# Kernel optimization log

Measured on AMD Instinct MI355X. Metric: run time of the kernel, lower is better.

The kernel has to match this reference:

```python
import jax, jax.numpy as jnp
import numpy as np

B, S, D = 4, 2048, 512
H, HD, RL = 8, 64, 64   # nheads, head_dim = D//H, rl_dim
TEMPER = 1.0
BETA = 1.0
SLOPE = 0.01  # LeakyReLU negative slope
LN_EPS = 1e-5


def setup_inputs() -> dict:
    key = jax.random.key(0)
    ks = jax.random.split(key, 12)
    scale = 0.02
    return {
        "h":   jax.random.normal(ks[0], (B, S, D), dtype=jnp.float32),
        "rh":  jax.random.normal(ks[1], (B, S, RL), dtype=jnp.float32),
        "Wl":  jax.random.normal(ks[2], (D, D), dtype=jnp.float32) * scale,   # linear_l (in,out)
        "Wr":  jax.random.normal(ks[3], (D, D), dtype=jnp.float32) * scale,   # linear_r
        "al":  jax.random.normal(ks[4], (HD,), dtype=jnp.float32) * scale,    # att_l: Linear(head_dim,1)
        "ar":  jax.random.normal(ks[5], (HD,), dtype=jnp.float32) * scale,    # att_r
        "Wrs": jax.random.normal(ks[6], (RL, RL * H), dtype=jnp.float32) * scale,  # r_source
        "Wrt": jax.random.normal(ks[7], (RL, RL * H), dtype=jnp.float32) * scale,  # r_target
        "Wf":  jax.random.normal(ks[8], (D, D), dtype=jnp.float32) * scale,   # linear_final
        "ln_g": jnp.ones((D,), dtype=jnp.float32),
        "ln_b": jnp.zeros((D,), dtype=jnp.float32),
    }


def _layer_norm(x, g, b):
    mu = jnp.mean(x, axis=-1, keepdims=True)
    var = jnp.mean(jnp.square(x - mu), axis=-1, keepdims=True)
    return (x - mu) * jax.lax.rsqrt(var + LN_EPS) * g + b


def reference(h, rh, Wl, Wr, al, ar, Wrs, Wrt, Wf, ln_g, ln_b):
    leaky = lambda x: jnp.where(x >= 0, x, SLOPE * x)
    # projections -> [B, H, S, HD]
    fl = (h @ Wl).reshape(B, S, H, HD).transpose(0, 2, 1, 3)
    fr = (h @ Wr).reshape(B, S, H, HD).transpose(0, 2, 1, 3)
    # additive attention logits: [B,H,S,1] + [B,H,1,S]
    sl = jnp.einsum('bhsd,d->bhs', leaky(fl), al)
    sr = jnp.einsum('bhsd,d->bhs', leaky(fr), ar)
    score = sl[:, :, :, None] + sr[:, :, None, :]
    # relation-embedding bilinear bias: r_k @ r_q -> [B,H,S,S]
    r_k = (rh @ Wrs).reshape(B, S, H, RL).transpose(0, 2, 1, 3)   # [B,H,S,RL]
    r_q = (rh @ Wrt).reshape(B, S, H, RL).transpose(0, 2, 3, 1)   # [B,H,RL,S]
    score = score + BETA * jnp.einsum('bhsr,bhrt->bhst', r_k, r_q)
    score = jax.nn.softmax(score / TEMPER, axis=-1)
    # context and output projection (dropout = 0 -> identity)
    context = jnp.einsum('bhst,bhtd->bhsd', score, fr)
    h_sa = context.transpose(0, 2, 1, 3).reshape(B, S, H * HD)
    fh = h_sa @ Wf
    return _layer_norm(h + fh, ln_g, ln_b)
```

## Files before the change

### kernel.cpp

```cpp
#include <hip/hip_runtime.h>
#include <math.h>

#define B_ 4
#define S_ 2048
#define D_ 512
#define H_ 8
#define HD_ 64
#define RL_ 64
#define LN_EPS 1e-5f
#define SLOPE 0.01f
#define LOG2E 1.4426950408889634f

typedef __attribute__((ext_vector_type(8))) __bf16 bf16x8;
typedef __attribute__((ext_vector_type(4))) float f32x4;

__device__ __forceinline__ float leaky(float x) { return x >= 0.f ? x : SLOPE * x; }

__device__ __forceinline__ ushort f2bf(float f) {
    union { float f; unsigned u; } v; v.f = f;
    unsigned r = v.u + 0x7fffu + ((v.u >> 16) & 1u);
    return (ushort)(r >> 16);
}
__device__ __forceinline__ unsigned fbits(float f) {
    union { float f; unsigned u; } v; v.f = f; return v.u;
}

__device__ __forceinline__ void g2lds16(const void* g, void* l) {
    __builtin_amdgcn_global_load_lds(
        (const __attribute__((address_space(1))) void*)(uintptr_t)g,
        (__attribute__((address_space(3))) void*)(uintptr_t)l, 16, 0, 0);
}

__global__ __launch_bounds__(256) void prep(
    const float* __restrict__ h, const float* __restrict__ rh,
    const float* __restrict__ Wr, const float* __restrict__ Wf,
    const float* __restrict__ Wrs, const float* __restrict__ Wrt,
    ushort* __restrict__ hb, ushort* __restrict__ rhb,
    ushort* __restrict__ WrT, ushort* __restrict__ WfT,
    ushort* __restrict__ WrsT, ushort* __restrict__ WrtT)
{
    const int bx = blockIdx.x, tid = threadIdx.x;
    if (bx < 4608) {
        const float* in = (bx < 4096) ? h : rh;
        ushort* o = (bx < 4096) ? hb : rhb;
        const int i = (bx < 4096 ? bx : bx - 4096) * 256 + tid;
        const float4 v = ((const float4*)in)[i];
        ushort4 u; u.x = f2bf(v.x); u.y = f2bf(v.y); u.z = f2bf(v.z); u.w = f2bf(v.w);
        ((ushort4*)o)[i] = u;
        return;
    }
    __shared__ float TS[64][65];
    int t = bx - 4608;
    const float* in; ushort* out; int K, tk, tn;
    if (t < 64)       { in = Wr;  out = WrT;  K = 512; tk = t & 7; tn = t >> 3; }
    else if (t < 128) { in = Wf;  out = WfT;  K = 512; t -= 64; tk = t & 7; tn = t >> 3; }
    else if (t < 136) { in = Wrs; out = WrsT; K = 64;  tk = 0; tn = t - 128; }
    else              { in = Wrt; out = WrtT; K = 64;  tk = 0; tn = t - 136; }
    const int k0 = tk * 64, n0 = tn * 64;
    const int r = tid >> 4, c4 = (tid & 15) * 4;
    #pragma unroll
    for (int p = 0; p < 4; ++p) {
        const int row = r + 16 * p;
        const float4 v = *(const float4*)(in + (size_t)(k0 + row) * 512 + n0 + c4);
        TS[row][c4] = v.x; TS[row][c4 + 1] = v.y;
        TS[row][c4 + 2] = v.z; TS[row][c4 + 3] = v.w;
    }
    __syncthreads();
    #pragma unroll
    for (int p = 0; p < 4; ++p) {
        const int nn = r + 16 * p;
        ushort4 o;
        o.x = f2bf(TS[c4 + 0][nn]); o.y = f2bf(TS[c4 + 1][nn]);
        o.z = f2bf(TS[c4 + 2][nn]); o.w = f2bf(TS[c4 + 3][nn]);
        *(ushort4*)(out + (size_t)(n0 + nn) * K + k0 + c4) = o;
    }
}

__global__ __launch_bounds__(256) void proj(
    const ushort* __restrict__ hb, const ushort* __restrict__ rhb,
    const ushort* __restrict__ WrT, const ushort* __restrict__ WrsT,
    const ushort* __restrict__ WrtT,
    ushort* __restrict__ frT, ushort* __restrict__ rkw, ushort* __restrict__ rqw,
    float* __restrict__ sred, const float* __restrict__ ar)
{
    __shared__ ushort As[2][64 * 32];
    __shared__ ushort Bs[2][128 * 32];

    const int tid = threadIdx.x;
    const int lane = tid & 63, w = tid >> 6;
    const int ln = lane & 15, quad = lane >> 4;
    const int wm = w >> 1, wn = w & 1;
    const int m0 = blockIdx.x * 64, n0 = blockIdx.y * 128;
    const int z = blockIdx.z;

    const ushort* A; const ushort* wt; ushort* co; float scl; int K;
    if (z == 0)      { A = hb;  wt = WrT;  co = frT; scl = LOG2E; K = 512; }
    else if (z == 1) { A = rhb; wt = WrsT; co = rkw; scl = LOG2E; K = 64; }
    else             { A = rhb; wt = WrtT; co = rqw; scl = 1.0f;  K = 64; }

    const int srA = tid >> 2;
    const int lchA = ((lane & 3) - (srA >> 1)) & 3;
    const ushort* AgB = A + (size_t)(m0 + srA) * K + lchA * 8;
    const int srB = w * 32 + (lane >> 2);
    const int lchB = ((lane & 3) - (srB >> 1)) & 3;
    const ushort* BgB0 = wt + (size_t)(n0 + srB) * K + lchB * 8;
    const ushort* BgB1 = BgB0 + (size_t)16 * K;
    const int aoff = tid * 8;
    const int boff = srB * 32 + (lane & 3) * 8;
    const int pc = (quad + (ln >> 1)) & 3;

    g2lds16(AgB, &As[0][aoff]);
    g2lds16(BgB0, &Bs[0][boff]);
    g2lds16(BgB1, &Bs[0][boff + 512]);

    f32x4 acc[2][4] = {};
    int buf = 0;
    for (int k0 = 0; k0 < K; k0 += 32) {
        __syncthreads();
        if (k0 + 32 < K) {
            g2lds16(AgB + k0 + 32, &As[buf ^ 1][aoff]);
            g2lds16(BgB0 + k0 + 32, &Bs[buf ^ 1][boff]);
            g2lds16(BgB1 + k0 + 32, &Bs[buf ^ 1][boff + 512]);
        }
        bf16x8 af[2], bfr[4];
        #pragma unroll
        for (int mi = 0; mi < 2; ++mi)
            af[mi] = *(const bf16x8*)&As[buf][(wm * 32 + mi * 16 + ln) * 32 + pc * 8];
        #pragma unroll
        for (int ni = 0; ni < 4; ++ni)
            bfr[ni] = *(const bf16x8*)&Bs[buf][(wn * 64 + ni * 16 + ln) * 32 + pc * 8];
        #pragma unroll
        for (int mi = 0; mi < 2; ++mi)
            #pragma unroll
            for (int ni = 0; ni < 4; ++ni)
                acc[mi][ni] = __builtin_amdgcn_mfma_f32_16x16x32_bf16(
                    af[mi], bfr[ni], acc[mi][ni], 0, 0, 0);
        buf ^= 1;
    }

    const int head = blockIdx.y * 2 + wn;
    const int b = m0 >> 11;
    const size_t bh = (size_t)b * H_ + head;
    if (z == 0) {
        #pragma unroll
        for (int mi = 0; mi < 2; ++mi) {
            const int s = (m0 & (S_ - 1)) + wm * 32 + mi * 16 + quad * 4;
            #pragma unroll
            for (int ni = 0; ni < 4; ++ni) {
                const int d = ni * 16 + ln;
                ushort4 o;
                o.x = f2bf(acc[mi][ni][0]); o.y = f2bf(acc[mi][ni][1]);
                o.z = f2bf(acc[mi][ni][2]); o.w = f2bf(acc[mi][ni][3]);
                *(ushort4*)(co + (bh * 64 + d) * S_ + s) = o;
            }
        }
        float a4[4];
        #pragma unroll
        for (int ni = 0; ni < 4; ++ni) a4[ni] = ar[ni * 16 + ln];
        #pragma unroll
        for (int mi = 0; mi < 2; ++mi) {
            const int s = (m0 & (S_ - 1)) + wm * 32 + mi * 16 + quad * 4;
            #pragma unroll
            for (int r = 0; r < 4; ++r) {
                float v = 0.f;
                #pragma unroll
                for (int ni = 0; ni < 4; ++ni)
                    v += leaky(acc[mi][ni][r]) * a4[ni];
                #pragma unroll
                for (int off = 8; off; off >>= 1) v += __shfl_xor(v, off, 16);
                if (ln == 0) sred[bh * S_ + s + r] = v * scl;
            }
        }
    } else {
        #pragma unroll
        for (int mi = 0; mi < 2; ++mi) {
            const int s = (m0 & (S_ - 1)) + wm * 32 + mi * 16 + quad * 4;
            #pragma unroll
            for (int ni = 0; ni < 4; ++ni) {
                const int d = ni * 16 + ln;
                #pragma unroll
                for (int r = 0; r < 4; ++r)
                    co[(bh * S_ + s + r) * 64 + d] = f2bf(acc[mi][ni][r] * scl);
            }
        }
    }
}

__global__ __launch_bounds__(256, 2) void attn_mfma(
    const ushort* __restrict__ frT, const ushort* __restrict__ rk,
    const ushort* __restrict__ rq, const float* __restrict__ sr,
    ushort* __restrict__ hsa)
{
    __shared__ ushort RQ[2][64][64];
    __shared__ ushort FT[2][64][64];
    __shared__ ushort PS[8][16][64];

    const int tid = threadIdx.x;
    const int w = tid >> 6;
    const int lane = tid & 63;
    const int ln = lane & 15;
    const int quad = lane >> 4;
    const int b = blockIdx.z, h = blockIdx.y, q0 = blockIdx.x * 128;
    const size_t bh = (size_t)b * H_ + h;

    bf16x8 a[2][2];
    #pragma unroll
    for (int qs = 0; qs < 2; ++qs) {
        const ushort* p = rk + ((bh * S_ + q0 + 32 * w + 16 * qs + ln) << 6);
        a[qs][0] = *(const bf16x8*)(p + quad * 8);
        a[qs][1] = *(const bf16x8*)(p + 32 + quad * 8);
    }

    const ushort* rq_g = rq + (bh * S_ << 6);
    const ushort* ft_g = frT + (size_t)bh * 64 * S_;
    const float* srp = sr + bh * S_;

    const int rl = lane >> 3;
    const int pg = lane & 7;
    const int row_b = w * 16 + rl;
    const int sgF = (pg - rl) & 7;
    const int sgR0 = (pg - 4 * w - (rl >> 2)) & 7;
    const int sgR1 = (pg - 4 * w - 2 - (rl >> 2)) & 7;

    #define STAGE(BUF, t0)                                                    \
        {                                                                     \
            g2lds16(rq_g + ((size_t)((t0) + row_b) << 6) + sgR0 * 8,          \
                    &RQ[BUF][row_b][pg * 8]);                                 \
            g2lds16(rq_g + ((size_t)((t0) + row_b + 8) << 6) + sgR1 * 8,      \
                    &RQ[BUF][row_b + 8][pg * 8]);                             \
            g2lds16(ft_g + (size_t)row_b * S_ + (t0) + sgF * 8,               \
                    &FT[BUF][row_b][pg * 8]);                                 \
            g2lds16(ft_g + (size_t)(row_b + 8) * S_ + (t0) + sgF * 8,         \
                    &FT[BUF][row_b + 8][pg * 8]);                             \
        }

    const ushort* rqrA = &RQ[0][0][0] + 4 * ln * 64 + ((quad + ln) & 7) * 8;
    const ushort* rqrB = &RQ[0][0][0] + 4 * ln * 64 + ((quad + 4 + ln) & 7) * 8;
    const ushort* ftrA = &FT[0][0][0] + ln * 64 + ((quad + ln) & 7) * 8;
    const ushort* ftrB = &FT[0][0][0] + ln * 64 + ((quad + 4 + ln) & 7) * 8;
    ushort* sb[2];
    sb[0] = &PS[w * 2][0][0]; sb[1] = &PS[w * 2 + 1][0][0];
    int wr_off[4];
    #pragma unroll
    for (int r = 0; r < 4; ++r) {
        const int prow = quad * 4 + r;
        wr_off[r] = prow * 64 + (((ln >> 1) + prow) & 7) * 8 + (ln & 1) * 4;
    }
    const int rd0 = ln * 64 + ((quad + ln) & 7) * 8;
    const int rd1 = ln * 64 + ((quad + 4 + ln) & 7) * 8;

    STAGE(0, 0)
    __syncthreads();

    float lsum[2][4] = {};
    f32x4 ctx[2][4] = {};

    for (int t0 = 0; t0 < S_; t0 += 128) {
        #pragma unroll
        for (int half = 0; half < 2; ++half) {
            const int tc = t0 + 64 * half;
            if (tc + 64 < S_) {
                if (half == 0) STAGE(1, tc + 64)
                else           STAGE(0, tc + 64)
            }
            const float4 srv = *(const float4*)(srp + tc + 4 * ln);

            f32x4 sc[2][4];
            #pragma unroll
            for (int jb = 0; jb < 4; ++jb) {
                const bf16x8 b0 = *(const bf16x8*)(rqrA + half * 4096 + jb * 64);
                const bf16x8 b1 = *(const bf16x8*)(rqrB + half * 4096 + jb * 64);
                #pragma unroll
                for (int qs = 0; qs < 2; ++qs) {
                    f32x4 t = {0.f, 0.f, 0.f, 0.f};
                    t = __builtin_amdgcn_mfma_f32_16x16x32_bf16(a[qs][0], b0, t, 0, 0, 0);
                    t = __builtin_amdgcn_mfma_f32_16x16x32_bf16(a[qs][1], b1, t, 0, 0, 0);
                    sc[qs][jb] = t;
                }
            }

            #pragma unroll
            for (int qs = 0; qs < 2; ++qs)
                #pragma unroll
                for (int r = 0; r < 4; ++r) {
                    const float p0 = __builtin_amdgcn_exp2f(sc[qs][0][r] + srv.x);
                    const float p1 = __builtin_amdgcn_exp2f(sc[qs][1][r] + srv.y);
                    const float p2 = __builtin_amdgcn_exp2f(sc[qs][2][r] + srv.z);
                    const float p3 = __builtin_amdgcn_exp2f(sc[qs][3][r] + srv.w);
                    lsum[qs][r] += (p0 + p1) + (p2 + p3);
                    const unsigned lo = (fbits(p0) >> 16) | (fbits(p1) & 0xffff0000u);
                    const unsigned hi = (fbits(p2) >> 16) | (fbits(p3) & 0xffff0000u);
                    *(uint2*)(sb[qs] + wr_off[r]) = make_uint2(lo, hi);
                }

            const bf16x8 pa00 = *(const bf16x8*)(sb[0] + rd0);
            const bf16x8 pa01 = *(const bf16x8*)(sb[0] + rd1);
            const bf16x8 pa10 = *(const bf16x8*)(sb[1] + rd0);
            const bf16x8 pa11 = *(const bf16x8*)(sb[1] + rd1);
            #pragma unroll
            for (int jb = 0; jb < 4; ++jb) {
                const bf16x8 fb0 = *(const bf16x8*)(ftrA + half * 4096 + jb * 1024);
                const bf16x8 fb1 = *(const bf16x8*)(ftrB + half * 4096 + jb * 1024);
                ctx[0][jb] = __builtin_amdgcn_mfma_f32_16x16x32_bf16(pa00, fb0, ctx[0][jb], 0, 0, 0);
                ctx[0][jb] = __builtin_amdgcn_mfma_f32_16x16x32_bf16(pa01, fb1, ctx[0][jb], 0, 0, 0);
                ctx[1][jb] = __builtin_amdgcn_mfma_f32_16x16x32_bf16(pa10, fb0, ctx[1][jb], 0, 0, 0);
                ctx[1][jb] = __builtin_amdgcn_mfma_f32_16x16x32_bf16(pa11, fb1, ctx[1][jb], 0, 0, 0);
            }

            __syncthreads();
        }
    }

    #pragma unroll
    for (int qs = 0; qs < 2; ++qs)
        #pragma unroll
        for (int r = 0; r < 4; ++r) {
            float l = lsum[qs][r];
            #pragma unroll
            for (int off = 8; off; off >>= 1) l += __shfl_xor(l, off, 16);
            const float inv = 1.f / l;
            const int q = q0 + 32 * w + 16 * qs + quad * 4 + r;
            ushort* orow = hsa + (size_t)(b * S_ + q) * D_ + h * 64;
            #pragma unroll
            for (int jb = 0; jb < 4; ++jb)
                orow[16 * jb + ln] = f2bf(ctx[qs][jb][r] * inv);
        }
}

__global__ __launch_bounds__(256) void gemm_out(
    const ushort* __restrict__ A, const ushort* __restrict__ WT,
    float* __restrict__ C)
{
    __shared__ ushort As[2][64 * 32];
    __shared__ ushort Bs[2][128 * 32];

    const int tid = threadIdx.x;
    const int lane = tid & 63, w = tid >> 6;
    const int ln = lane & 15, quad = lane >> 4;
    const int wm = w >> 1, wn = w & 1;
    const int m0 = blockIdx.x * 64, n0 = blockIdx.y * 128;
    const int K = 512;

    const int srA = tid >> 2;
    const int lchA = ((lane & 3) - (srA >> 1)) & 3;
    const ushort* AgB = A + (size_t)(m0 + srA) * K + lchA * 8;
    const int srB = w * 32 + (lane >> 2);
    const int lchB = ((lane & 3) - (srB >> 1)) & 3;
    const ushort* BgB0 = WT + (size_t)(n0 + srB) * K + lchB * 8;
    const ushort* BgB1 = BgB0 + (size_t)16 * K;
    const int aoff = tid * 8;
    const int boff = srB * 32 + (lane & 3) * 8;
    const int pc = (quad + (ln >> 1)) & 3;

    g2lds16(AgB, &As[0][aoff]);
    g2lds16(BgB0, &Bs[0][boff]);
    g2lds16(BgB1, &Bs[0][boff + 512]);

    f32x4 acc[2][4] = {};
    int buf = 0;
    for (int k0 = 0; k0 < K; k0 += 32) {
        __syncthreads();
        if (k0 + 32 < K) {
            g2lds16(AgB + k0 + 32, &As[buf ^ 1][aoff]);
            g2lds16(BgB0 + k0 + 32, &Bs[buf ^ 1][boff]);
            g2lds16(BgB1 + k0 + 32, &Bs[buf ^ 1][boff + 512]);
        }
        bf16x8 af[2], bfr[4];
        #pragma unroll
        for (int mi = 0; mi < 2; ++mi)
            af[mi] = *(const bf16x8*)&As[buf][(wm * 32 + mi * 16 + ln) * 32 + pc * 8];
        #pragma unroll
        for (int ni = 0; ni < 4; ++ni)
            bfr[ni] = *(const bf16x8*)&Bs[buf][(wn * 64 + ni * 16 + ln) * 32 + pc * 8];
        #pragma unroll
        for (int mi = 0; mi < 2; ++mi)
            #pragma unroll
            for (int ni = 0; ni < 4; ++ni)
                acc[mi][ni] = __builtin_amdgcn_mfma_f32_16x16x32_bf16(
                    af[mi], bfr[ni], acc[mi][ni], 0, 0, 0);
        buf ^= 1;
    }

    #pragma unroll
    for (int mi = 0; mi < 2; ++mi) {
        const int row = m0 + wm * 32 + mi * 16 + quad * 4;
        #pragma unroll
        for (int ni = 0; ni < 4; ++ni) {
            const int col = n0 + wn * 64 + ni * 16 + ln;
            #pragma unroll
            for (int r = 0; r < 4; ++r)
                C[(size_t)(row + r) * 512 + col] = acc[mi][ni][r];
        }
    }
}

__global__ __launch_bounds__(256) void ln_kernel(
    const float* __restrict__ h, const float* __restrict__ fh,
    const float* __restrict__ g, const float* __restrict__ bb,
    float* __restrict__ out)
{
    const int row = blockIdx.x, tid = threadIdx.x;
    const float* hp = h + (size_t)row * 512;
    const float* fp = fh + (size_t)row * 512;
    const float x0 = hp[tid] + fp[tid];
    const float x1 = hp[tid + 256] + fp[tid + 256];
    __shared__ float red[4];

    float s = x0 + x1;
    #pragma unroll
    for (int off = 32; off; off >>= 1) s += __shfl_xor(s, off, 64);
    if ((tid & 63) == 0) red[tid >> 6] = s;
    __syncthreads();
    const float mu = (red[0] + red[1] + red[2] + red[3]) * (1.f / 512.f);

    const float d0 = x0 - mu, d1 = x1 - mu;
    float v = d0 * d0 + d1 * d1;
    #pragma unroll
    for (int off = 32; off; off >>= 1) v += __shfl_xor(v, off, 64);
    __syncthreads();
    if ((tid & 63) == 0) red[tid >> 6] = v;
    __syncthreads();
    const float var = (red[0] + red[1] + red[2] + red[3]) * (1.f / 512.f);
    const float inv = rsqrtf(var + LN_EPS);

    out[(size_t)row * 512 + tid] = d0 * inv * g[tid] + bb[tid];
    out[(size_t)row * 512 + tid + 256] = d1 * inv * g[tid + 256] + bb[tid + 256];
}

extern "C" void kernel_launch(void* const* d_in, const int* in_sizes, int n_in,
                              void* d_out, int out_size, void* d_ws, size_t ws_size,
                              hipStream_t stream)
{
    const float* h   = (const float*)d_in[0];
    const float* rh  = (const float*)d_in[1];
    const float* Wr  = (const float*)d_in[3];
    const float* ar  = (const float*)d_in[5];
    const float* Wrs = (const float*)d_in[6];
    const float* Wrt = (const float*)d_in[7];
    const float* Wf  = (const float*)d_in[8];
    const float* lng = (const float*)d_in[9];
    const float* lnb = (const float*)d_in[10];
    float* out = (float*)d_out;
    char* wsb  = (char*)d_ws;

    const size_t MB = (size_t)1 << 20;
    ushort* hb   = (ushort*)(wsb);
    ushort* rhb  = (ushort*)(wsb + 8 * MB);
    ushort* WrT  = (ushort*)(wsb + 9 * MB);
    ushort* WfT  = (ushort*)(wsb + 9 * MB + 512 * 1024);
    ushort* WrsT = (ushort*)(wsb + 10 * MB);
    ushort* WrtT = (ushort*)(wsb + 10 * MB + 64 * 1024);
    ushort* frT  = (ushort*)(wsb + 11 * MB);
    ushort* rkw  = (ushort*)(wsb + 19 * MB);
    ushort* rqw  = (ushort*)(wsb + 27 * MB);
    float*  sr   = (float*) (wsb + 35 * MB);
    ushort* hsab = (ushort*)(wsb + 36 * MB);
    float*  fh   = (float*) (wsb + 44 * MB);

    dim3 blk(256);
    prep<<<dim3(4752), blk, 0, stream>>>(h, rh, Wr, Wf, Wrs, Wrt,
                                         hb, rhb, WrT, WfT, WrsT, WrtT);
    proj<<<dim3(128, 4, 3), blk, 0, stream>>>(hb, rhb, WrT, WrsT, WrtT,
                                              frT, rkw, rqw, sr, ar);
    attn_mfma<<<dim3(S_ / 128, H_, B_), blk, 0, stream>>>(frT, rkw, rqw, sr, hsab);
    gemm_out<<<dim3(128, 4), blk, 0, stream>>>(hsab, WfT, fh);
    ln_kernel<<<dim3(B_ * S_), blk, 0, stream>>>(h, fh, lng, lnb, out);
}
```

Before: 175.5 us.

## Fuse output GEMM with residual LayerNorm; load A fragments directly from global

Replaces the separate output-projection GEMM and LayerNorm kernels with one kernel where each block computes 32 full rows of 512 columns, adds the residual and does the row-normalisation in registers with a shared-memory reduction. This removes the fp32 intermediate write and read of fh and one launch. It also loads A-operand MFMA fragments straight from global memory into registers, in both proj and the new kernel, dropping the A shared-memory staging. The trade-off is a grid of only 256 large blocks with big LDS use and launch_bounds(…,1), which lowers occupancy. Variance is now computed as E[x²]−mu² in one pass, which is slightly less numerically robust.

```diff
diff --git a/kernel.cpp b/kernel.cpp
--- a/kernel.cpp
+++ b/kernel.cpp
@@ -83,7 +83,6 @@
     ushort* __restrict__ frT, ushort* __restrict__ rkw, ushort* __restrict__ rqw,
     float* __restrict__ sred, const float* __restrict__ ar)
 {
-    __shared__ ushort As[2][64 * 32];
     __shared__ ushort Bs[2][128 * 32];
 
     const int tid = threadIdx.x;
@@ -98,34 +97,33 @@
     else if (z == 1) { A = rhb; wt = WrsT; co = rkw; scl = LOG2E; K = 64; }
     else             { A = rhb; wt = WrtT; co = rqw; scl = 1.0f;  K = 64; }
 
-    const int srA = tid >> 2;
-    const int lchA = ((lane & 3) - (srA >> 1)) & 3;
-    const ushort* AgB = A + (size_t)(m0 + srA) * K + lchA * 8;
     const int srB = w * 32 + (lane >> 2);
     const int lchB = ((lane & 3) - (srB >> 1)) & 3;
     const ushort* BgB0 = wt + (size_t)(n0 + srB) * K + lchB * 8;
     const ushort* BgB1 = BgB0 + (size_t)16 * K;
-    const int aoff = tid * 8;
     const int boff = srB * 32 + (lane & 3) * 8;
     const int pc = (quad + (ln >> 1)) & 3;
 
-    g2lds16(AgB, &As[0][aoff]);
+    const ushort* Ar0 = A + (size_t)(m0 + wm * 32 + ln) * K + quad * 8;
+    const ushort* Ar1 = A + (size_t)(m0 + wm * 32 + 16 + ln) * K + quad * 8;
+
     g2lds16(BgB0, &Bs[0][boff]);
     g2lds16(BgB1, &Bs[0][boff + 512]);
+    bf16x8 a_cur[2], a_nxt[2];
+    a_cur[0] = *(const bf16x8*)Ar0;
+    a_cur[1] = *(const bf16x8*)Ar1;
 
     f32x4 acc[2][4] = {};
     int buf = 0;
     for (int k0 = 0; k0 < K; k0 += 32) {
         __syncthreads();
         if (k0 + 32 < K) {
-            g2lds16(AgB + k0 + 32, &As[buf ^ 1][aoff]);
             g2lds16(BgB0 + k0 + 32, &Bs[buf ^ 1][boff]);
             g2lds16(BgB1 + k0 + 32, &Bs[buf ^ 1][boff + 512]);
-        }
-        bf16x8 af[2], bfr[4];
-        #pragma unroll
-        for (int mi = 0; mi < 2; ++mi)
-            af[mi] = *(const bf16x8*)&As[buf][(wm * 32 + mi * 16 + ln) * 32 + pc * 8];
+            a_nxt[0] = *(const bf16x8*)(Ar0 + k0 + 32);
+            a_nxt[1] = *(const bf16x8*)(Ar1 + k0 + 32);
+        }
+        bf16x8 bfr[4];
         #pragma unroll
         for (int ni = 0; ni < 4; ++ni)
             bfr[ni] = *(const bf16x8*)&Bs[buf][(wn * 64 + ni * 16 + ln) * 32 + pc * 8];
@@ -134,7 +132,8 @@
             #pragma unroll
             for (int ni = 0; ni < 4; ++ni)
                 acc[mi][ni] = __builtin_amdgcn_mfma_f32_16x16x32_bf16(
-                    af[mi], bfr[ni], acc[mi][ni], 0, 0, 0);
+                    a_cur[mi], bfr[ni], acc[mi][ni], 0, 0, 0);
+        a_cur[0] = a_nxt[0]; a_cur[1] = a_nxt[1];
         buf ^= 1;
     }
 
@@ -327,104 +326,112 @@
         }
 }
 
-__global__ __launch_bounds__(256) void gemm_out(
+__global__ __launch_bounds__(256, 1) void gemm_ln(
     const ushort* __restrict__ A, const ushort* __restrict__ WT,
-    float* __restrict__ C)
+    const float* __restrict__ h, const float* __restrict__ g,
+    const float* __restrict__ bb, float* __restrict__ out)
 {
-    __shared__ ushort As[2][64 * 32];
-    __shared__ ushort Bs[2][128 * 32];
+    __shared__ ushort Bs[2][512 * 32];
+    __shared__ float red[32][8];
 
     const int tid = threadIdx.x;
     const int lane = tid & 63, w = tid >> 6;
     const int ln = lane & 15, quad = lane >> 4;
-    const int wm = w >> 1, wn = w & 1;
-    const int m0 = blockIdx.x * 64, n0 = blockIdx.y * 128;
-    const int K = 512;
-
-    const int srA = tid >> 2;
-    const int lchA = ((lane & 3) - (srA >> 1)) & 3;
-    const ushort* AgB = A + (size_t)(m0 + srA) * K + lchA * 8;
-    const int srB = w * 32 + (lane >> 2);
-    const int lchB = ((lane & 3) - (srB >> 1)) & 3;
-    const ushort* BgB0 = WT + (size_t)(n0 + srB) * K + lchB * 8;
-    const ushort* BgB1 = BgB0 + (size_t)16 * K;
-    const int aoff = tid * 8;
-    const int boff = srB * 32 + (lane & 3) * 8;
-    const int pc = (quad + (ln >> 1)) & 3;
-
-    g2lds16(AgB, &As[0][aoff]);
-    g2lds16(BgB0, &Bs[0][boff]);
-    g2lds16(BgB1, &Bs[0][boff + 512]);
-
-    f32x4 acc[2][4] = {};
+    const int m0 = blockIdx.x * 32;
+
+    const int srow = lane >> 2;
+    const int pch = lane & 3;
+    const int lg = (pch - (srow & 3) - ((srow >> 2) & 3)) & 3;
+    const ushort* Bg[8];
+    uint bo[8];
+    #pragma unroll
+    for (int i = 0; i < 8; ++i) {
+        const int nrow = w * 128 + i * 16 + srow;
+        Bg[i] = WT + (size_t)nrow * 512 + lg * 8;
+        bo[i] = (w * 128 + i * 16) * 32 + lane * 8;
+    }
+    const int prc = (quad + (ln & 3) + ((ln >> 2) & 3)) & 3;
+
+    const ushort* Ar0 = A + (size_t)(m0 + ln) * 512 + quad * 8;
+    const ushort* Ar1 = A + (size_t)(m0 + 16 + ln) * 512 + quad * 8;
+
+    #pragma unroll
+    for (int i = 0; i < 8; ++i) g2lds16(Bg[i], &Bs[0][bo[i]]);
+    bf16x8 a_cur[2], a_nxt[2];
+    a_cur[0] = *(const bf16x8*)Ar0;
+    a_cur[1] = *(const bf16x8*)Ar1;
+
+    f32x4 acc[2][8] = {};
     int buf = 0;
-    for (int k0 = 0; k0 < K; k0 += 32) {
+    for (int k0 = 0; k0 < 512; k0 += 32) {
         __syncthreads();
-        if (k0 + 32 < K) {
-            g2lds16(AgB + k0 + 32, &As[buf ^ 1][aoff]);
-            g2lds16(BgB0 + k0 + 32, &Bs[buf ^ 1][boff]);
-            g2lds16(BgB1 + k0 + 32, &Bs[buf ^ 1][boff + 512]);
-        }
-        bf16x8 af[2], bfr[4];
-        #pragma unroll
-        for (int mi = 0; mi < 2; ++mi)
-            af[mi] = *(const bf16x8*)&As[buf][(wm * 32 + mi * 16 + ln) * 32 + pc * 8];
-        #pragma unroll
-        for (int ni = 0; ni < 4; ++ni)
-            bfr[ni] = *(const bf16x8*)&Bs[buf][(wn * 64 + ni * 16 + ln) * 32 + pc * 8];
-        #pragma unroll
-        for (int mi = 0; mi < 2; ++mi)
-            #pragma unroll
-            for (int ni = 0; ni < 4; ++ni)
-                acc[mi][ni] = __builtin_amdgcn_mfma_f32_16x16x32_bf16(
-                    af[mi], bfr[ni], acc[mi][ni], 0, 0, 0);
+        if (k0 + 32 < 512) {
+            #pragma unroll
+            for (int i = 0; i < 8; ++i) g2lds16(Bg[i] + k0 + 32, &Bs[buf ^ 1][bo[i]]);
+            a_nxt[0] = *(const bf16x8*)(Ar0 + k0 + 32);
+            a_nxt[1] = *(const bf16x8*)(Ar1 + k0 + 32);
+        }
+        #pragma unroll
+        for (int ni = 0; ni < 8; ++ni) {
+            const bf16x8 bf = *(const bf16x8*)&Bs[buf][(w * 128 + ni * 16 + ln) * 32 + prc * 8];
+            acc[0][ni] = __builtin_amdgcn_mfma_f32_16x16x32_bf16(a_cur[0], bf, acc[0][ni], 0, 0, 0);
+            acc[1][ni] = __builtin_amdgcn_mfma_f32_16x16x32_bf16(a_cur[1], bf, acc[1][ni], 0, 0, 0);
+        }
+        a_cur[0] = a_nxt[0]; a_cur[1] = a_nxt[1];
         buf ^= 1;
     }
 
     #pragma unroll
-    for (int mi = 0; mi < 2; ++mi) {
-        const int row = m0 + wm * 32 + mi * 16 + quad * 4;
-        #pragma unroll
-        for (int ni = 0; ni < 4; ++ni) {
-            const int col = n0 + wn * 64 + ni * 16 + ln;
-            #pragma unroll
-            for (int r = 0; r < 4; ++r)
-                C[(size_t)(row + r) * 512 + col] = acc[mi][ni][r];
-        }
-    }
-}
-
-__global__ __launch_bounds__(256) void ln_kernel(
-    const float* __restrict__ h, const float* __restrict__ fh,
-    const float* __restrict__ g, const float* __restrict__ bb,
-    float* __restrict__ out)
-{
-    const int row = blockIdx.x, tid = threadIdx.x;
-    const float* hp = h + (size_t)row * 512;
-    const float* fp = fh + (size_t)row * 512;
-    const float x0 = hp[tid] + fp[tid];
-    const float x1 = hp[tid + 256] + fp[tid + 256];
-    __shared__ float red[4];
-
-    float s = x0 + x1;
-    #pragma unroll
-    for (int off = 32; off; off >>= 1) s += __shfl_xor(s, off, 64);
-    if ((tid & 63) == 0) red[tid >> 6] = s;
+    for (int mi = 0; mi < 2; ++mi)
+        #pragma unroll
+        for (int r = 0; r < 4; ++r) {
+            const int row = m0 + mi * 16 + quad * 4 + r;
+            #pragma unroll
+            for (int ni = 0; ni < 8; ++ni)
+                acc[mi][ni][r] += h[(size_t)row * 512 + w * 128 + ni * 16 + ln];
+        }
+    #pragma unroll
+    for (int mi = 0; mi < 2; ++mi)
+        #pragma unroll
+        for (int r = 0; r < 4; ++r) {
+            float s = 0.f, s2 = 0.f;
+            #pragma unroll
+            for (int ni = 0; ni < 8; ++ni) {
+                const float x = acc[mi][ni][r];
+                s += x; s2 += x * x;
+            }
+            #pragma unroll
+            for (int off = 8; off; off >>= 1) {
+                s += __shfl_xor(s, off, 16);
+                s2 += __shfl_xor(s2, off, 16);
+            }
+            if (ln == 0) {
+                red[mi * 16 + quad * 4 + r][w * 2] = s;
+                red[mi * 16 + quad * 4 + r][w * 2 + 1] = s2;
+            }
+        }
     __syncthreads();
-    const float mu = (red[0] + red[1] + red[2] + red[3]) * (1.f / 512.f);
-
-    const float d0 = x0 - mu, d1 = x1 - mu;
-    float v = d0 * d0 + d1 * d1;
-    #pragma unroll
-    for (int off = 32; off; off >>= 1) v += __shfl_xor(v, off, 64);
-    __syncthreads();
-    if ((tid & 63) == 0) red[tid >> 6] = v;
-    __syncthreads();
-    const float var = (red[0] + red[1] + red[2] + red[3]) * (1.f / 512.f);
-    const float inv = rsqrtf(var + LN_EPS);
-
-    out[(size_t)row * 512 + tid] = d0 * inv * g[tid] + bb[tid];
-    out[(size_t)row * 512 + tid + 256] = d1 * inv * g[tid + 256] + bb[tid + 256];
+
+    float gv[8], bv[8];
+    #pragma unroll
+    for (int ni = 0; ni < 8; ++ni) {
+        gv[ni] = g[w * 128 + ni * 16 + ln];
+        bv[ni] = bb[w * 128 + ni * 16 + ln];
+    }
+    #pragma unroll
+    for (int mi = 0; mi < 2; ++mi)
+        #pragma unroll
+        for (int r = 0; r < 4; ++r) {
+            const int lrow = mi * 16 + quad * 4 + r;
+            const float S  = red[lrow][0] + red[lrow][2] + red[lrow][4] + red[lrow][6];
+            const float S2 = red[lrow][1] + red[lrow][3] + red[lrow][5] + red[lrow][7];
+            const float mu = S * (1.f / 512.f);
+            const float inv = rsqrtf(S2 * (1.f / 512.f) - mu * mu + LN_EPS);
+            const size_t rb = (size_t)(m0 + lrow) * 512 + w * 128;
+            #pragma unroll
+            for (int ni = 0; ni < 8; ++ni)
+                out[rb + ni * 16 + ln] = (acc[mi][ni][r] - mu) * inv * gv[ni] + bv[ni];
+        }
 }
 
 extern "C" void kernel_launch(void* const* d_in, const int* in_sizes, int n_in,
@@ -455,7 +462,6 @@
     ushort* rqw  = (ushort*)(wsb + 27 * MB);
     float*  sr   = (float*) (wsb + 35 * MB);
     ushort* hsab = (ushort*)(wsb + 36 * MB);
-    float*  fh   = (float*) (wsb + 44 * MB);
 
     dim3 blk(256);
     prep<<<dim3(4752), blk, 0, stream>>>(h, rh, Wr, Wf, Wrs, Wrt,
@@ -463,6 +469,5 @@
     proj<<<dim3(128, 4, 3), blk, 0, stream>>>(hb, rhb, WrT, WrsT, WrtT,
                                               frT, rkw, rqw, sr, ar);
     attn_mfma<<<dim3(S_ / 128, H_, B_), blk, 0, stream>>>(frT, rkw, rqw, sr, hsab);
-    gemm_out<<<dim3(128, 4), blk, 0, stream>>>(hsab, WfT, fh);
-    ln_kernel<<<dim3(B_ * S_), blk, 0, stream>>>(h, fh, lng, lnb, out);
-}
+    gemm_ln<<<dim3(256), blk, 0, stream>>>(hsab, WfT, h, lng, lnb, out);
+}
```

New measurement: 179.2 us. +2.1%, slower.
